# Kernel optimization log

Measured on AMD Instinct MI355X. Metric: run time of the kernel, lower is better.

Reference implementation:

```python
import jax, jax.numpy as jnp
import numpy as np

B, D, T = 16, 256, 4096
K = 1024
COMMITMENT_COST = 0.25


def setup_inputs() -> dict:
    key = jax.random.key(0)
    k1, k2 = jax.random.split(key)
    z = jax.random.normal(k1, (B, D, T), dtype=jnp.float32)
    # codebook initialized uniform(-1/K, 1/K) as in the torch module
    embeddings = jax.random.uniform(k2, (K, D), dtype=jnp.float32,
                                    minval=-1.0 / K, maxval=1.0 / K)
    return {"z": z, "embeddings": embeddings}


def reference(z, embeddings):
    # z: (B, D, T) -> (B, T, D)
    zt = jnp.transpose(z, (0, 2, 1))
    flat_z = zt.reshape(-1, D)  # (N, D), N = B*T
    # squared L2 distances to every codebook entry: (N, K)
    distances = (jnp.sum(flat_z * flat_z, axis=1, keepdims=True)
                 + jnp.sum(embeddings * embeddings, axis=1)
                 - 2.0 * flat_z @ embeddings.T)
    indices = jnp.argmin(distances, axis=1)  # (N,)
    # gather replaces the one-hot @ embeddings matmul (same result)
    quantized = embeddings[indices].reshape(B, T, D)
    # commitment loss (quantized detached)
    e_latent_loss = jnp.mean((jax.lax.stop_gradient(quantized) - zt) ** 2)
    loss = COMMITMENT_COST * e_latent_loss
    # straight-through estimator
    quantized_ste = zt + jax.lax.stop_gradient(quantized - zt)
    # perplexity from mean of one-hot encodings = normalized code histogram
    counts = jnp.zeros((K,), dtype=jnp.float32).at[indices].add(1.0)
    avg_probs = counts / flat_z.shape[0]
    perplexity = jnp.exp(-jnp.sum(avg_probs * jnp.log(avg_probs + 1e-10)))
    out = jnp.transpose(quantized_ste, (0, 2, 1))  # (B, D, T)
    return out, indices.reshape(B, T), loss, perplexity
```

## Files before the change

### kernel.cpp

```cpp
#include <hip/hip_runtime.h>
#include <hip/hip_bf16.h>

#define BB 16
#define DDIM 256
#define TLEN 4096
#define KCODES 1024
#define NQ (BB*TLEN)
#define QB 64
#define MAXC 32
#define DELTA 4e-4f

#define FLT_MAX_C 3.402823466e+38f

using short8 = __attribute__((ext_vector_type(8))) short;
using f32x4  = __attribute__((ext_vector_type(4))) float;

__device__ __forceinline__ unsigned short f2bf(float x) {
  unsigned u = __float_as_uint(x);
  unsigned r = (u + 0x7fffu + ((u >> 16) & 1u)) >> 16;
  return (unsigned short)r;
}
__device__ __forceinline__ float bf2f(unsigned short h) {
  return __uint_as_float(((unsigned)h) << 16);
}

__device__ __forceinline__ float np_sumsq_256(const float* p, int stride) {
  float th[2];
#pragma unroll
  for (int h = 0; h < 2; ++h) {
    const float* q = p + (size_t)h * 128 * (size_t)stride;
    float r[8];
#pragma unroll
    for (int j = 0; j < 8; ++j) {
      float v = q[(size_t)j * (size_t)stride];
      r[j] = __fmul_rn(v, v);
    }
    for (int i = 8; i < 128; i += 8) {
#pragma unroll
      for (int j = 0; j < 8; ++j) {
        float v = q[(size_t)(i + j) * (size_t)stride];
        r[j] = __fadd_rn(r[j], __fmul_rn(v, v));
      }
    }
    th[h] = __fadd_rn(__fadd_rn(__fadd_rn(r[0], r[1]), __fadd_rn(r[2], r[3])),
                      __fadd_rn(__fadd_rn(r[4], r[5]), __fadd_rn(r[6], r[7])));
  }
  return __fadd_rn(th[0], th[1]);
}

__global__ void k_prep(const float* __restrict__ emb, float* __restrict__ embT,
                       float* __restrict__ e2, short* __restrict__ ebh,
                       short* __restrict__ ebl) {
  const int k = blockIdx.x;
  const int d = threadIdx.x;
  __shared__ float row[DDIM];
  float v = emb[(size_t)k * DDIM + d];
  row[d] = v;
  embT[(size_t)d * KCODES + k] = v;
  unsigned short h = f2bf(v);
  ebh[(size_t)k * DDIM + d] = (short)h;
  ebl[(size_t)k * DDIM + d] = (short)f2bf(v - bf2f(h));
  __syncthreads();
  if (d == 0) e2[k] = np_sumsq_256(row, 1);
}

__global__ __launch_bounds__(512, 2)
void k_mdist(const float* __restrict__ z, const float* __restrict__ emb,
             const short* __restrict__ ebh, const short* __restrict__ ebl,
             const float* __restrict__ e2, int* __restrict__ idx,
             int* __restrict__ hist, double* __restrict__ lossp) {
  extern __shared__ __align__(16) char sbuf[];
  float*  zf  = (float*)sbuf;
  short8* abh = (short8*)(sbuf + 65536);
  short8* abl = (short8*)(sbuf + 98304);
  float* z2s  = (float*)(sbuf + 65536);
  float* sm   = (float*)(sbuf + 65536 + 256);
  float* qmin = (float*)(sbuf + 65536 + 2304);
  int*   cnt  = (int*)(sbuf + 65536 + 2560);
  int*   ovf  = (int*)(sbuf + 65536 + 2816);
  int*   cand = (int*)(sbuf + 65536 + 3072);
  float* bd   = (float*)(sbuf + 65536 + 11264);
  int*   bk   = (int*)(sbuf + 65536 + 13312);

  const int tid = threadIdx.x;
  const int lane = tid & 63;
  const int w = tid >> 6;
  const int g = lane >> 4;
  const int c = lane & 15;
  const int n0 = blockIdx.x * QB;
  const int kb = w * 128;
  const float* zp = z + (size_t)(n0 >> 12) * DDIM * TLEN + (n0 & (TLEN - 1));

#pragma unroll
  for (int i = 0; i < 8; ++i) {
    int s4 = i * 512 + tid;
    int d = s4 >> 4, q4 = (s4 & 15) * 4;
    *(float4*)&zf[d * QB + q4] = *(const float4*)(zp + (size_t)d * TLEN + q4);
  }
  __syncthreads();

#pragma unroll
  for (int i = 0; i < 4; ++i) {
    int s = i * 512 + tid;
    int ks = s >> 8, mt = (s >> 6) & 3, ln = s & 63;
    int q = mt * 16 + (ln & 15);
    int d0 = ks * 32 + (ln >> 4) * 8;
    short8 h, l;
#pragma unroll
    for (int j = 0; j < 8; ++j) {
      float v = zf[(d0 + j) * QB + q];
      unsigned short hh = f2bf(v);
      h[j] = (short)hh;
      l[j] = (short)f2bf(v - bf2f(hh));
    }
    abh[s] = h;
    abl[s] = l;
  }
  __syncthreads();

  f32x4 acc[4][8];
#pragma unroll
  for (int mt = 0; mt < 4; ++mt)
#pragma unroll
    for (int nt = 0; nt < 8; ++nt) {
      f32x4 zz = {0.f, 0.f, 0.f, 0.f};
      acc[mt][nt] = zz;
    }

  const size_t lbase = (size_t)(kb + c) * DDIM + g * 8;
  const short* ebp_h = ebh + lbase;
  const short* ebp_l = ebl + lbase;
  short8 pbh = *(const short8*)(ebp_h);
  short8 pbl = *(const short8*)(ebp_l);

  for (int ks = 0; ks < 8; ++ks) {
    short8 ah[4], al[4];
#pragma unroll
    for (int mt = 0; mt < 4; ++mt) {
      ah[mt] = abh[ks * 256 + mt * 64 + lane];
      al[mt] = abl[ks * 256 + mt * 64 + lane];
    }
#pragma unroll
    for (int nt = 0; nt < 8; ++nt) {
      short8 bh = pbh, bl = pbl;
      if (!(ks == 7 && nt == 7)) {
        int nm = ks * 8 + nt + 1;
        size_t off = (size_t)(nm & 7) * (16 * DDIM) + (size_t)(nm >> 3) * 32;
        pbh = *(const short8*)(ebp_h + off);
        pbl = *(const short8*)(ebp_l + off);
      }
#pragma unroll
      for (int mt = 0; mt < 4; ++mt) {
        acc[mt][nt] = __builtin_amdgcn_mfma_f32_16x16x32_bf16(ah[mt], bh, acc[mt][nt], 0, 0, 0);
        acc[mt][nt] = __builtin_amdgcn_mfma_f32_16x16x32_bf16(al[mt], bh, acc[mt][nt], 0, 0, 0);
        acc[mt][nt] = __builtin_amdgcn_mfma_f32_16x16x32_bf16(ah[mt], bl, acc[mt][nt], 0, 0, 0);
      }
    }
  }
  __syncthreads();

  if (tid < QB) {
    z2s[tid] = np_sumsq_256(&zf[tid], QB);
    cnt[tid] = 0;
    ovf[tid] = 0;
  }

  float e2c[8];
#pragma unroll
  for (int nt = 0; nt < 8; ++nt) e2c[nt] = e2[kb + nt * 16 + c];

  float smin[4][4];
#pragma unroll
  for (int mt = 0; mt < 4; ++mt)
#pragma unroll
    for (int r = 0; r < 4; ++r) {
      float m = FLT_MAX_C;
#pragma unroll
      for (int nt = 0; nt < 8; ++nt)
        m = fminf(m, e2c[nt] - 2.0f * acc[mt][nt][r]);
      smin[mt][r] = m;
    }
#pragma unroll
  for (int mt = 0; mt < 4; ++mt)
#pragma unroll
    for (int r = 0; r < 4; ++r) {
#pragma unroll
      for (int m = 1; m < 16; m <<= 1)
        smin[mt][r] = fminf(smin[mt][r], __shfl_xor(smin[mt][r], m, 64));
    }
  if (c == 0) {
#pragma unroll
    for (int mt = 0; mt < 4; ++mt)
#pragma unroll
      for (int r = 0; r < 4; ++r)
        sm[w * QB + mt * 16 + g * 4 + r] = smin[mt][r];
  }
  __syncthreads();
  if (tid < QB) {
    float m = sm[tid];
#pragma unroll
    for (int wv = 1; wv < 8; ++wv) m = fminf(m, sm[wv * QB + tid]);
    qmin[tid] = m;
  }
  __syncthreads();

#pragma unroll
  for (int mt = 0; mt < 4; ++mt)
#pragma unroll
    for (int r = 0; r < 4; ++r) {
      const int ql = mt * 16 + g * 4 + r;
      const float lim = qmin[ql] + DELTA;
#pragma unroll
      for (int nt = 0; nt < 8; ++nt) {
        float s = e2c[nt] - 2.0f * acc[mt][nt][r];
        if (s <= lim) {
          int p = atomicAdd(&cnt[ql], 1);
          if (p < MAXC) cand[ql * MAXC + p] = kb + nt * 16 + c;
          else ovf[ql] = 1;
        }
      }
    }
  __syncthreads();

  {
    const int q = tid & 63;
    const int slot = tid >> 6;
    const float z2q = z2s[q];
    float bestd = FLT_MAX_C;
    int besti = (1 << 30);
    const bool all = (ovf[q] != 0) || (cnt[q] > MAXC);
    const int count = all ? KCODES : cnt[q];
    for (int ci = slot; ci < count; ci += 8) {
      const int k = all ? ci : cand[q * MAXC + ci];
      const float4* ek = (const float4*)(emb + (size_t)k * DDIM);
      float a0 = 0.f;
      for (int dd = 0; dd < 64; ++dd) {
        float4 e4 = ek[dd];
        a0 = __fmaf_rn(zf[(dd * 4 + 0) * QB + q], e4.x, a0);
        a0 = __fmaf_rn(zf[(dd * 4 + 1) * QB + q], e4.y, a0);
        a0 = __fmaf_rn(zf[(dd * 4 + 2) * QB + q], e4.z, a0);
        a0 = __fmaf_rn(zf[(dd * 4 + 3) * QB + q], e4.w, a0);
      }
      float dist = __fsub_rn(__fadd_rn(z2q, e2[k]), __fmul_rn(2.0f, a0));
      if (dist < bestd || (dist == bestd && k < besti)) { bestd = dist; besti = k; }
    }
    bd[q * 8 + slot] = bestd;
    bk[q * 8 + slot] = besti;
  }
  __syncthreads();

  if (tid < QB) {
    float B = bd[tid * 8 + 0];
    int K = bk[tid * 8 + 0];
#pragma unroll
    for (int s = 1; s < 8; ++s) {
      float d2 = bd[tid * 8 + s];
      int k2 = bk[tid * 8 + s];
      if (d2 < B || (d2 == B && k2 < K)) { B = d2; K = k2; }
    }
    idx[n0 + tid] = K;
    atomicAdd(&hist[K], 1);
    double ls = (double)B;
#pragma unroll
    for (int m = 1; m < 64; m <<= 1) ls += __shfl_xor(ls, m, 64);
    if (tid == 0) lossp[blockIdx.x] = ls;
  }
}

__global__ void k_idxout(const int* __restrict__ idx,
                         float* __restrict__ oidx) {
  int n = blockIdx.x * 256 + threadIdx.x;
  oidx[n] = (float)(idx[n] & (KCODES - 1));
}

__global__ void k_gather(const float* __restrict__ embT,
                         const int* __restrict__ idx,
                         float* __restrict__ out) {
  __shared__ float er[KCODES];
  const int blk = blockIdx.x;
  const int bq = blk >> 8;
  const int d = blk & 255;
  const int tid = threadIdx.x;
  *((float4*)&er[tid * 4]) =
      *((const float4*)(embT + (size_t)d * KCODES + tid * 4));
  __syncthreads();
  const int* ip = idx + (size_t)bq * TLEN;
  float* op = out + (size_t)blk * TLEN;
#pragma unroll
  for (int c = 0; c < 16; ++c) {
    int t = c * 256 + tid;
    int kk = ip[t] & (KCODES - 1);
    op[t] = er[kk];
  }
}

__global__ void k_final(const int* __restrict__ hist,
                        const double* __restrict__ lossp,
                        float* __restrict__ out2) {
  const int tid = threadIdx.x;
  double ls = 0.0;
  for (int i = 0; i < 4; ++i) ls += lossp[tid * 4 + i];
  float es = 0.f;
  for (int i = tid; i < KCODES; i += 256) {
    float p = (float)hist[i] / 65536.0f;
    es += p * logf(p + 1e-10f);
  }
#pragma unroll
  for (int m = 1; m < 64; m <<= 1) {
    ls += __shfl_xor(ls, m, 64);
    es += __shfl_xor(es, m, 64);
  }
  __shared__ double lw[4];
  __shared__ float ew[4];
  if ((tid & 63) == 0) { lw[tid >> 6] = ls; ew[tid >> 6] = es; }
  __syncthreads();
  if (tid == 0) {
    double lt = lw[0] + lw[1] + lw[2] + lw[3];
    float et = ew[0] + ew[1] + ew[2] + ew[3];
    float loss = 0.25f * (float)(lt / (double)((long long)NQ * DDIM));
    float perp = expf(-et);
    out2[0] = loss;
    out2[1] = perp;
  }
}

extern "C" void kernel_launch(void* const* d_in, const int* in_sizes, int n_in,
                              void* d_out, int out_size, void* d_ws, size_t ws_size,
                              hipStream_t stream) {
  const float* z = (const float*)d_in[0];
  const float* emb = (const float*)d_in[1];
  float* out = (float*)d_out;

  char* ws = (char*)d_ws;
  float* embT = (float*)(ws);
  float* e2 = (float*)(ws + 1048576);
  int* idx = (int*)(ws + 1052672);
  int* hist = (int*)(ws + 1314816);
  double* lossp = (double*)(ws + 1318912);
  short* ebh = (short*)(ws + 1327104);
  short* ebl = (short*)(ws + 1851392);

  float* oidx = out + ((size_t)out_size - 2 - NQ);
  float* out2 = out + ((size_t)out_size - 2);

  (void)hipFuncSetAttribute((const void*)k_mdist,
                            hipFuncAttributeMaxDynamicSharedMemorySize,
                            131072);

  hipMemsetAsync(hist, 0, KCODES * sizeof(int), stream);

  k_prep<<<KCODES, 256, 0, stream>>>(emb, embT, e2, ebh, ebl);
  k_mdist<<<NQ / QB, 512, 131072, stream>>>(z, emb, ebh, ebl, e2, idx, hist,
                                            lossp);
  k_idxout<<<NQ / 256, 256, 0, stream>>>(idx, oidx);
  k_gather<<<BB * DDIM, 256, 0, stream>>>(embT, idx, out);
  k_final<<<1, 256, 0, stream>>>(hist, lossp, out2);
}
```

Measured before the change: 228.3 us.

## Use single bf16 MFMA with error-bounded candidate margin for distance screening

Replaces the three-term split-bf16 MFMA (hi*hi, lo*hi, hi*lo) with a single bf16 product per tile, removing the low-part codebook and z buffers. To keep argmin exact, the candidate threshold becomes an error bound that scales with the maximum codebook magnitude and each query's L1 norm, and k_prep computes that maximum with an atomic. This cuts MFMA work by about two thirds and reduces shared memory to 96KB, but launch bounds drop to one block per CU. Wider margins may push more queries into the candidate-overflow path and the exact-rescoring stage.

Result: no change. 230.6 us (+1.0%).

```diff
diff --git a/kernel.cpp b/kernel.cpp
--- a/kernel.cpp
+++ b/kernel.cpp
@@ -8,7 +8,6 @@
 #define NQ (BB*TLEN)
 #define QB 64
 #define MAXC 32
-#define DELTA 4e-4f
 
 #define FLT_MAX_C 3.402823466e+38f
 
@@ -50,37 +49,39 @@
 
 __global__ void k_prep(const float* __restrict__ emb, float* __restrict__ embT,
                        float* __restrict__ e2, short* __restrict__ ebh,
-                       short* __restrict__ ebl) {
+                       unsigned* __restrict__ maxe) {
   const int k = blockIdx.x;
   const int d = threadIdx.x;
   __shared__ float row[DDIM];
   float v = emb[(size_t)k * DDIM + d];
   row[d] = v;
   embT[(size_t)d * KCODES + k] = v;
-  unsigned short h = f2bf(v);
-  ebh[(size_t)k * DDIM + d] = (short)h;
-  ebl[(size_t)k * DDIM + d] = (short)f2bf(v - bf2f(h));
+  ebh[(size_t)k * DDIM + d] = (short)f2bf(v);
+  float a = fabsf(v);
+#pragma unroll
+  for (int m = 1; m < 64; m <<= 1) a = fmaxf(a, __shfl_xor(a, m, 64));
+  if ((threadIdx.x & 63) == 0) atomicMax(maxe, __float_as_uint(a));
   __syncthreads();
   if (d == 0) e2[k] = np_sumsq_256(row, 1);
 }
 
-__global__ __launch_bounds__(512, 2)
+__global__ __launch_bounds__(512, 1)
 void k_mdist(const float* __restrict__ z, const float* __restrict__ emb,
-             const short* __restrict__ ebh, const short* __restrict__ ebl,
-             const float* __restrict__ e2, int* __restrict__ idx,
+             const short* __restrict__ ebh, const float* __restrict__ e2,
+             const unsigned* __restrict__ maxeU, int* __restrict__ idx,
              int* __restrict__ hist, double* __restrict__ lossp) {
   extern __shared__ __align__(16) char sbuf[];
   float*  zf  = (float*)sbuf;
   short8* abh = (short8*)(sbuf + 65536);
-  short8* abl = (short8*)(sbuf + 98304);
   float* z2s  = (float*)(sbuf + 65536);
-  float* sm   = (float*)(sbuf + 65536 + 256);
-  float* qmin = (float*)(sbuf + 65536 + 2304);
-  int*   cnt  = (int*)(sbuf + 65536 + 2560);
-  int*   ovf  = (int*)(sbuf + 65536 + 2816);
-  int*   cand = (int*)(sbuf + 65536 + 3072);
-  float* bd   = (float*)(sbuf + 65536 + 11264);
-  int*   bk   = (int*)(sbuf + 65536 + 13312);
+  float* sabs = (float*)(sbuf + 65536 + 256);
+  float* sm   = (float*)(sbuf + 65536 + 512);
+  float* qmin = (float*)(sbuf + 65536 + 2560);
+  int*   cnt  = (int*)(sbuf + 65536 + 2816);
+  int*   ovf  = (int*)(sbuf + 65536 + 3072);
+  int*   cand = (int*)(sbuf + 65536 + 3328);
+  float* bd   = (float*)(sbuf + 65536 + 11520);
+  int*   bk   = (int*)(sbuf + 65536 + 13568);
 
   const int tid = threadIdx.x;
   const int lane = tid & 63;
@@ -105,16 +106,10 @@
     int ks = s >> 8, mt = (s >> 6) & 3, ln = s & 63;
     int q = mt * 16 + (ln & 15);
     int d0 = ks * 32 + (ln >> 4) * 8;
-    short8 h, l;
-#pragma unroll
-    for (int j = 0; j < 8; ++j) {
-      float v = zf[(d0 + j) * QB + q];
-      unsigned short hh = f2bf(v);
-      h[j] = (short)hh;
-      l[j] = (short)f2bf(v - bf2f(hh));
-    }
+    short8 h;
+#pragma unroll
+    for (int j = 0; j < 8; ++j) h[j] = (short)f2bf(zf[(d0 + j) * QB + q]);
     abh[s] = h;
-    abl[s] = l;
   }
   __syncthreads();
 
@@ -127,43 +122,39 @@
       acc[mt][nt] = zz;
     }
 
-  const size_t lbase = (size_t)(kb + c) * DDIM + g * 8;
-  const short* ebp_h = ebh + lbase;
-  const short* ebp_l = ebl + lbase;
-  short8 pbh = *(const short8*)(ebp_h);
-  short8 pbl = *(const short8*)(ebp_l);
+  const short* ebp = ebh + (size_t)(kb + c) * DDIM + g * 8;
+  short8 pb0 = *(const short8*)(ebp);
+  short8 pb1 = *(const short8*)(ebp + 16 * DDIM);
 
   for (int ks = 0; ks < 8; ++ks) {
-    short8 ah[4], al[4];
-#pragma unroll
-    for (int mt = 0; mt < 4; ++mt) {
-      ah[mt] = abh[ks * 256 + mt * 64 + lane];
-      al[mt] = abl[ks * 256 + mt * 64 + lane];
-    }
+    short8 ah[4];
+#pragma unroll
+    for (int mt = 0; mt < 4; ++mt) ah[mt] = abh[ks * 256 + mt * 64 + lane];
 #pragma unroll
     for (int nt = 0; nt < 8; ++nt) {
-      short8 bh = pbh, bl = pbl;
-      if (!(ks == 7 && nt == 7)) {
-        int nm = ks * 8 + nt + 1;
-        size_t off = (size_t)(nm & 7) * (16 * DDIM) + (size_t)(nm >> 3) * 32;
-        pbh = *(const short8*)(ebp_h + off);
-        pbl = *(const short8*)(ebp_l + off);
-      }
-#pragma unroll
-      for (int mt = 0; mt < 4; ++mt) {
-        acc[mt][nt] = __builtin_amdgcn_mfma_f32_16x16x32_bf16(ah[mt], bh, acc[mt][nt], 0, 0, 0);
-        acc[mt][nt] = __builtin_amdgcn_mfma_f32_16x16x32_bf16(al[mt], bh, acc[mt][nt], 0, 0, 0);
-        acc[mt][nt] = __builtin_amdgcn_mfma_f32_16x16x32_bf16(ah[mt], bl, acc[mt][nt], 0, 0, 0);
-      }
+      short8 bh = (nt & 1) ? pb1 : pb0;
+      int m = (ks * 8 + nt + 2) & 63;
+      size_t off = (size_t)(m & 7) * (16 * DDIM) + (size_t)(m >> 3) * 32;
+      short8 nv = *(const short8*)(ebp + off);
+      if (nt & 1) pb1 = nv; else pb0 = nv;
+#pragma unroll
+      for (int mt = 0; mt < 4; ++mt)
+        acc[mt][nt] =
+            __builtin_amdgcn_mfma_f32_16x16x32_bf16(ah[mt], bh, acc[mt][nt], 0, 0, 0);
     }
   }
   __syncthreads();
 
   if (tid < QB) {
     z2s[tid] = np_sumsq_256(&zf[tid], QB);
+    float sa = 0.f;
+    for (int d = 0; d < DDIM; ++d) sa += fabsf(zf[d * QB + tid]);
+    sabs[tid] = sa;
     cnt[tid] = 0;
     ovf[tid] = 0;
   }
+
+  const float maxe = __uint_as_float(*maxeU);
 
   float e2c[8];
 #pragma unroll
@@ -209,7 +200,7 @@
 #pragma unroll
     for (int r = 0; r < 4; ++r) {
       const int ql = mt * 16 + g * 4 + r;
-      const float lim = qmin[ql] + DELTA;
+      const float lim = qmin[ql] + (maxe * sabs[ql]) * 0.009f + 2e-4f;
 #pragma unroll
       for (int nt = 0; nt < 8; ++nt) {
         float s = e2c[nt] - 2.0f * acc[mt][nt][r];
@@ -336,22 +327,22 @@
   float* e2 = (float*)(ws + 1048576);
   int* idx = (int*)(ws + 1052672);
   int* hist = (int*)(ws + 1314816);
-  double* lossp = (double*)(ws + 1318912);
-  short* ebh = (short*)(ws + 1327104);
-  short* ebl = (short*)(ws + 1851392);
+  unsigned* maxe = (unsigned*)(ws + 1318912);
+  double* lossp = (double*)(ws + 1318920);
+  short* ebh = (short*)(ws + 1327120);
 
   float* oidx = out + ((size_t)out_size - 2 - NQ);
   float* out2 = out + ((size_t)out_size - 2);
 
   (void)hipFuncSetAttribute((const void*)k_mdist,
                             hipFuncAttributeMaxDynamicSharedMemorySize,
-                            131072);
-
-  hipMemsetAsync(hist, 0, KCODES * sizeof(int), stream);
-
-  k_prep<<<KCODES, 256, 0, stream>>>(emb, embT, e2, ebh, ebl);
-  k_mdist<<<NQ / QB, 512, 131072, stream>>>(z, emb, ebh, ebl, e2, idx, hist,
-                                            lossp);
+                            98304);
+
+  hipMemsetAsync(hist, 0, KCODES * sizeof(int) + sizeof(unsigned), stream);
+
+  k_prep<<<KCODES, 256, 0, stream>>>(emb, embT, e2, ebh, maxe);
+  k_mdist<<<NQ / QB, 512, 98304, stream>>>(z, emb, ebh, e2, maxe, idx, hist,
+                                           lossp);
   k_idxout<<<NQ / 256, 256, 0, stream>>>(idx, oidx);
   k_gather<<<BB * DDIM, 256, 0, stream>>>(embT, idx, out);
   k_final<<<1, 256, 0, stream>>>(hist, lossp, out2);
```
